# Kernel optimization log

Measured on AMD Instinct MI355X. Metric: run time of the kernel, lower is better.

## Reference

```python
import jax, jax.numpy as jnp
import numpy as np

# nuScenes-scale config: batch 2, 360x360 BEV grid (1440/4), 128 channels,
# 10 classes, 200 proposals, 3x3 NMS kernel, 40k occupied voxels per sample.
B, H, W_GRID, NUM_CLS, NUM_PROP, NMS_K = 2, 360, 360, 10, 200, 3
C = 128
N_PER_B = 40000
NEG_FILL = -1000000.0  # scatter_nd fill value from to_dense()


def _bev_pos():
    # replicates create_2D_grid: coord = (x_index_along_dim1, y_index_along_dim0)
    xs = jnp.arange(H, dtype=jnp.float32)
    ys = jnp.arange(W_GRID, dtype=jnp.float32)
    by, bx = jnp.meshgrid(xs, ys, indexing='ij')  # by[i,j]=i, bx[i,j]=j
    return jnp.stack([bx, by], axis=-1).reshape(-1, 2)  # [H*W, 2]


def setup_inputs() -> dict:
    key = jax.random.key(0)
    ks = jax.random.split(key, 10)
    # unique spatial locations per batch sample (sparse voxel coords)
    flats = [jax.random.permutation(ks[i], H * W_GRID)[:N_PER_B] for i in range(B)]
    flat = jnp.concatenate(flats)
    b = jnp.repeat(jnp.arange(B), N_PER_B)
    indices = jnp.stack([b, flat // W_GRID, flat % W_GRID], axis=1).astype(jnp.int32)
    features = jax.random.normal(ks[4], (B * N_PER_B, C), jnp.float32)
    # heatmap head (pointwise linears standing in for the submconv stack)
    W_hm1 = jax.random.normal(ks[5], (C, C), jnp.float32) * (2.0 / C) ** 0.5
    b_hm1 = jnp.zeros((C,), jnp.float32)
    W_hm2 = jax.random.normal(ks[6], (C, NUM_CLS), jnp.float32) * (2.0 / C) ** 0.5
    b_hm2 = jnp.full((NUM_CLS,), -2.19, jnp.float32)  # fc[-1].bias.fill_(-2.19)
    # class_encoding: nn.Conv1d(num_class, channels, 1)
    W_cls = jax.random.normal(ks[7], (C, NUM_CLS), jnp.float32) * 0.1
    b_cls = jnp.zeros((C,), jnp.float32)
    return dict(features=features, W_hm1=W_hm1, b_hm1=b_hm1, W_hm2=W_hm2,
                b_hm2=b_hm2, W_cls=W_cls, b_cls=b_cls, indices=indices)


def reference(features, W_hm1, b_hm1, W_hm2, b_hm2, W_cls, b_cls, indices):
    bidx, yi, xi = indices[:, 0], indices[:, 1], indices[:, 2]
    HW = H * W_GRID

    # --- x.dense(): scatter voxel features to dense BEV grid (zero fill) ---
    xd = jnp.zeros((B, H, W_GRID, C), features.dtype).at[bidx, yi, xi].set(features)
    x_flat = xd.reshape(B, HW, C).transpose(0, 2, 1)  # [B, C, HW]

    # --- heatmap head (per-voxel) then to_dense() with -1e6 fill ---
    hm = jax.nn.relu(features @ W_hm1 + b_hm1) @ W_hm2 + b_hm2  # [N, NUM_CLS]
    dense_hm = jnp.full((B, H, W_GRID, NUM_CLS), NEG_FILL, hm.dtype)
    dense_hm = dense_hm.at[bidx, yi, xi].set(hm).transpose(0, 3, 1, 2)  # [B,K,H,W]

    heat = jax.nn.sigmoid(dense_hm)  # detached in original

    # --- NMS-kernel peak extraction ---
    pad = NMS_K // 2
    inner = jax.lax.reduce_window(heat, -jnp.inf, jax.lax.max,
                                  (1, 1, NMS_K, NMS_K), (1, 1, 1, 1), 'VALID')
    local_max = jnp.zeros_like(heat).at[:, :, pad:H - pad, pad:W_GRID - pad].set(inner)
    # pedestrian (8) and traffic_cone (9): kernel size 1
    local_max = local_max.at[:, 8].set(heat[:, 8]).at[:, 9].set(heat[:, 9])
    heat = heat * (heat == local_max)
    heat_f = heat.reshape(B, NUM_CLS, HW)

    # --- top-k proposals over (class, location) ---
    _, top = jax.lax.top_k(heat_f.reshape(B, -1), NUM_PROP)  # [B, P]
    cls = top // HW
    idx = top % HW

    # --- gather proposal features + class encoding ---
    qf = jnp.take_along_axis(x_flat, jnp.broadcast_to(idx[:, None, :], (B, C, NUM_PROP)), axis=2)
    onehot = jax.nn.one_hot(cls, NUM_CLS, dtype=qf.dtype)  # [B, P, K]
    qf = qf + jnp.einsum('ck,bpk->bcp', W_cls, onehot) + b_cls[None, :, None]

    # --- proposal positions and heatmap scores ---
    query_pos = _bev_pos()[idx]  # [B, P, 2]
    qhs = jnp.take_along_axis(heat_f, jnp.broadcast_to(idx[:, None, :], (B, NUM_CLS, NUM_PROP)), axis=2)
    return qf, query_pos, qhs, cls
```

## Files before the change

### kernel.cpp

```cpp
#include <hip/hip_runtime.h>

#define HW 129600
#define WG 360
#define HG 360
#define NCLS 10
#define NPROP 200
#define CDIM 128
#define NROWS 80000
#define NB 2
#define NPB (NROWS / NB)
#define SEL_CAP 4096
#define HBINS 4096
#define RPB 64
#define PSTR 12

__device__ __forceinline__ void lds_cp16(float* l, const float* g) {
  __builtin_amdgcn_global_load_lds(
      (const __attribute__((address_space(1))) void*)g,
      (__attribute__((address_space(3))) void*)l, 16, 0, 0);
}

__device__ __forceinline__ float4 fmax4(float4 a, float4 b) {
  float4 r;
  r.x = fmaxf(a.x, b.x);
  r.y = fmaxf(a.y, b.y);
  r.z = fmaxf(a.z, b.z);
  r.w = fmaxf(a.w, b.w);
  return r;
}

__global__ __launch_bounds__(256, 4) void k_head(
    const float* __restrict__ feat, const float* __restrict__ W1,
    const float* __restrict__ b1, const float* __restrict__ W2,
    const float* __restrict__ b2, const int* __restrict__ idxs,
    float* __restrict__ val_raw, int* __restrict__ rowmap) {
  __shared__ __align__(16) float lds_w[2][16 * 128];
  __shared__ __align__(16) float lds_f[2][RPB * 16];
  const int tid = threadIdx.x;
  const int row0 = blockIdx.x * RPB;
  const int tc = tid & 31;
  const int tr = tid >> 5;
  const int wv = tid >> 6;
  const int lane = tid & 63;

  auto stage = [&](int kt, int nb) {
#pragma unroll
    for (int c = 0; c < 2; ++c) {
      const int off = (wv * 2 + c) * 256;
      lds_cp16(&lds_w[nb][off], W1 + kt * 2048 + off + lane * 4);
    }
    {
      const int off = wv * 256;
      const int fidx = off + lane * 4;
      const int r = fidx >> 4, kk = fidx & 15;
      lds_cp16(&lds_f[nb][off],
               feat + (size_t)(row0 + r) * CDIM + kt * 16 + kk);
    }
  };

  stage(0, 0);
  if (tid < RPB) {
    int row = row0 + tid;
    int bb = idxs[row * 3 + 0];
    int yy = idxs[row * 3 + 1];
    int xx = idxs[row * 3 + 2];
    rowmap[(size_t)bb * HW + yy * WG + xx] = row;
  }
  __syncthreads();

  float acc[8][4];
#pragma unroll
  for (int r = 0; r < 8; ++r)
#pragma unroll
    for (int c = 0; c < 4; ++c) acc[r][c] = 0.f;

  for (int kt = 0; kt < 8; ++kt) {
    const int cb = kt & 1;
    if (kt < 7) stage(kt + 1, cb ^ 1);
#pragma unroll
    for (int kg = 0; kg < 4; ++kg) {
      float4 w0 = *(const float4*)(&lds_w[cb][(kg * 4 + 0) * 128 + tc * 4]);
      float4 w1 = *(const float4*)(&lds_w[cb][(kg * 4 + 1) * 128 + tc * 4]);
      float4 w2 = *(const float4*)(&lds_w[cb][(kg * 4 + 2) * 128 + tc * 4]);
      float4 w3 = *(const float4*)(&lds_w[cb][(kg * 4 + 3) * 128 + tc * 4]);
#pragma unroll
      for (int r = 0; r < 8; ++r) {
        float4 fv = *(const float4*)(&lds_f[cb][(tr * 8 + r) * 16 + kg * 4]);
        acc[r][0] = fmaf(fv.x, w0.x, acc[r][0]);
        acc[r][0] = fmaf(fv.y, w1.x, acc[r][0]);
        acc[r][0] = fmaf(fv.z, w2.x, acc[r][0]);
        acc[r][0] = fmaf(fv.w, w3.x, acc[r][0]);
        acc[r][1] = fmaf(fv.x, w0.y, acc[r][1]);
        acc[r][1] = fmaf(fv.y, w1.y, acc[r][1]);
        acc[r][1] = fmaf(fv.z, w2.y, acc[r][1]);
        acc[r][1] = fmaf(fv.w, w3.y, acc[r][1]);
        acc[r][2] = fmaf(fv.x, w0.z, acc[r][2]);
        acc[r][2] = fmaf(fv.y, w1.z, acc[r][2]);
        acc[r][2] = fmaf(fv.z, w2.z, acc[r][2]);
        acc[r][2] = fmaf(fv.w, w3.z, acc[r][2]);
        acc[r][3] = fmaf(fv.x, w0.w, acc[r][3]);
        acc[r][3] = fmaf(fv.y, w1.w, acc[r][3]);
        acc[r][3] = fmaf(fv.z, w2.w, acc[r][3]);
        acc[r][3] = fmaf(fv.w, w3.w, acc[r][3]);
      }
    }
    __syncthreads();
  }

  float* w2t = &lds_f[0][0];
  for (int i = tid; i < CDIM * NCLS; i += 256) {
    int k = i / NCLS, j = i - k * NCLS;
    w2t[j * 128 + k] = W2[i];
  }
  __syncthreads();

  float* hbuf = &lds_w[0][0];
  float4 b1v = *(const float4*)(b1 + tc * 4);
#pragma unroll
  for (int half = 0; half < 2; ++half) {
    if ((tr >> 2) == half) {
      int ltr = tr & 3;
#pragma unroll
      for (int r = 0; r < 8; ++r) {
        float4 h;
        h.x = fmaxf(acc[r][0] + b1v.x, 0.f);
        h.y = fmaxf(acc[r][1] + b1v.y, 0.f);
        h.z = fmaxf(acc[r][2] + b1v.z, 0.f);
        h.w = fmaxf(acc[r][3] + b1v.w, 0.f);
        *(float4*)(hbuf + (ltr * 8 + r) * 128 + tc * 4) = h;
      }
    }
    __syncthreads();
    for (int o = tid; o < 32 * NCLS; o += 256) {
      int r = o / NCLS, j = o - r * NCLS;
      float s = b2[j];
      for (int i4 = 0; i4 < 32; ++i4) {
        int k4 = (i4 + tid) & 31;
        float4 hv = *(const float4*)(hbuf + r * 128 + k4 * 4);
        float4 wv2 = *(const float4*)(w2t + j * 128 + k4 * 4);
        s = fmaf(hv.x, wv2.x, s);
        s = fmaf(hv.y, wv2.y, s);
        s = fmaf(hv.z, wv2.z, s);
        s = fmaf(hv.w, wv2.w, s);
      }
      float heat = 1.0f / (1.0f + expf(-s));
      int gr = half * 32 + r;
      val_raw[(size_t)(row0 + gr) * PSTR + j] = heat;
    }
    __syncthreads();
  }
}

__global__ __launch_bounds__(256) void k_hist(
    const float* __restrict__ val_raw, const int* __restrict__ idxs,
    const int* __restrict__ rowmap, const float* __restrict__ zrow,
    float* __restrict__ val, unsigned int* __restrict__ hist) {
  __shared__ unsigned int lh[HBINS];
  const int tid = threadIdx.x;
  const int row = blockIdx.x * 256 + tid;
  const int blk_b = (blockIdx.x * 256 >= NPB) ? 1 : 0;
  for (int i = tid; i < HBINS; i += 256) lh[i] = 0;
  __syncthreads();

  float v[10];
  int bb = 0;
  const bool valid = row < NROWS;
  if (valid) {
    bb = (row >= NPB) ? 1 : 0;
    const int y = idxs[row * 3 + 1];
    const int x = idxs[row * 3 + 2];
    const int pos = y * WG + x;
    const float* cbase = val_raw + (size_t)row * PSTR;
    float4 c0 = *(const float4*)(cbase + 0);
    float4 c1 = *(const float4*)(cbase + 4);
    float2 c89 = *(const float2*)(cbase + 8);
    const bool interior = (y > 0 && y < HG - 1 && x > 0 && x < WG - 1);
    if (interior) {
      const int d[8] = {-1, 1, -WG - 1, -WG, -WG + 1, WG - 1, WG, WG + 1};
      float4 m0 = c0, m1 = c1;
      const int* rmb = rowmap + (size_t)bb * HW + pos;
#pragma unroll
      for (int n = 0; n < 8; ++n) {
        int nrow = rmb[d[n]];
        const float* p =
            (nrow >= 0) ? (val_raw + (size_t)nrow * PSTR) : zrow;
        m0 = fmax4(m0, *(const float4*)(p + 0));
        m1 = fmax4(m1, *(const float4*)(p + 4));
      }
      v[0] = (c0.x == m0.x) ? c0.x : 0.f;
      v[1] = (c0.y == m0.y) ? c0.y : 0.f;
      v[2] = (c0.z == m0.z) ? c0.z : 0.f;
      v[3] = (c0.w == m0.w) ? c0.w : 0.f;
      v[4] = (c1.x == m1.x) ? c1.x : 0.f;
      v[5] = (c1.y == m1.y) ? c1.y : 0.f;
      v[6] = (c1.z == m1.z) ? c1.z : 0.f;
      v[7] = (c1.w == m1.w) ? c1.w : 0.f;
    } else {
      v[0] = v[1] = v[2] = v[3] = v[4] = v[5] = v[6] = v[7] = 0.f;
    }
    v[8] = c89.x;
    v[9] = c89.y;
    float4 s0 = {v[0], v[1], v[2], v[3]};
    float4 s1 = {v[4], v[5], v[6], v[7]};
    float4 s2 = {v[8], v[9], 0.f, 0.f};
    *(float4*)(val + (size_t)row * PSTR + 0) = s0;
    *(float4*)(val + (size_t)row * PSTR + 4) = s1;
    *(float4*)(val + (size_t)row * PSTR + 8) = s2;
#pragma unroll
    for (int c = 0; c < 10; ++c) {
      if (v[c] > 0.f) {
        unsigned int bin = __float_as_uint(v[c]) >> 18;
        if (bb == blk_b)
          atomicAdd(&lh[bin], 1u);
        else
          atomicAdd(&hist[(size_t)bb * HBINS + bin], 1u);
      }
    }
  }
  __syncthreads();
  unsigned int* gh = hist + (size_t)blk_b * HBINS;
  for (int i = tid; i < HBINS; i += 256) {
    unsigned int c = lh[i];
    if (c) atomicAdd(&gh[i], c);
  }
}

__global__ __launch_bounds__(256) void k_collect(
    const float* __restrict__ val, const int* __restrict__ idxs,
    const unsigned int* __restrict__ hist, unsigned long long* __restrict__ sel,
    int* __restrict__ sel_cnt) {
  __shared__ unsigned int coarse[256];
  __shared__ int sT[2];
  const int tid = threadIdx.x;
  for (int bb = 0; bb < NB; ++bb) {
    const unsigned int* h = hist + (size_t)bb * HBINS;
    unsigned int s = 0;
#pragma unroll
    for (int i = 0; i < HBINS / 256; ++i) s += h[tid * (HBINS / 256) + i];
    coarse[tid] = s;
    __syncthreads();
    if (tid == 0) {
      unsigned int cum = 0;
      int T = 0;
      int ci = 255;
      for (; ci >= 0; --ci) {
        if (cum + coarse[ci] >= NPROP) break;
        cum += coarse[ci];
      }
      if (ci >= 0) {
        int t = 15;
        for (; t > 0; --t) {
          unsigned int c = h[ci * 16 + t];
          if (cum + c >= NPROP) break;
          cum += c;
        }
        T = ci * 16 + t;
      }
      sT[bb] = T;
    }
    __syncthreads();
  }
  const int row = blockIdx.x * 256 + tid;
  const bool valid = row < NROWS;
  const int bb = (valid && row >= NPB) ? 1 : 0;
  const int T = sT[bb];
  float v[12];
  int pos = 0;
  if (valid) {
    *(float4*)(v + 0) = *(const float4*)(val + (size_t)row * PSTR + 0);
    *(float4*)(v + 4) = *(const float4*)(val + (size_t)row * PSTR + 4);
    *(float4*)(v + 8) = *(const float4*)(val + (size_t)row * PSTR + 8);
    pos = idxs[row * 3 + 1] * WG + idxs[row * 3 + 2];
  }
  const int lane = tid & 63;
#pragma unroll
  for (int cl = 0; cl < 10; ++cl) {
    float vv = valid ? v[cl] : 0.f;
    unsigned int bits = __float_as_uint(vv);
    bool pred = (vv > 0.f) && ((int)(bits >> 18) >= T);
    unsigned long long m0 = __ballot(pred && (bb == 0));
    unsigned long long m1 = __ballot(pred && (bb == 1));
    if (pred) {
      unsigned long long mask = bb ? m1 : m0;
      int leader = __ffsll((unsigned long long)mask) - 1;
      int lb = __popcll(mask & ((1ull << lane) - 1ull));
      int base = 0;
      if (lane == leader) base = atomicAdd(&sel_cnt[bb], (int)__popcll(mask));
      base = __shfl(base, leader, 64);
      unsigned int gidx = (unsigned int)cl * HW + (unsigned int)pos;
      unsigned long long key =
          ((unsigned long long)bits << 32) | (unsigned long long)(~gidx);
      int slot = base + lb;
      if (slot < SEL_CAP) sel[(size_t)bb * SEL_CAP + slot] = key;
    }
  }
}

__global__ __launch_bounds__(256) void k_final(
    const unsigned long long* __restrict__ sel, const int* __restrict__ sel_cnt,
    const float* __restrict__ val, const int* __restrict__ rowmap,
    const float* __restrict__ feat, const float* __restrict__ Wc,
    const float* __restrict__ bc, float* __restrict__ out) {
  __shared__ unsigned long long sk[SEL_CAP];
  __shared__ unsigned long long winners[NPROP];
  __shared__ int wcls[NPROP];
  __shared__ int wrow[NPROP];
  const int b = blockIdx.x;
  const int tid = threadIdx.x;
  int M = sel_cnt[b];
  if (M > SEL_CAP) M = SEL_CAP;
  for (int i = tid; i < M; i += 256) sk[i] = sel[(size_t)b * SEL_CAP + i];
  __syncthreads();
  for (int i = tid; i < M; i += 256) {
    unsigned long long key = sk[i];
    int rank = 0;
    for (int j = 0; j < M; ++j) rank += (sk[j] > key) ? 1 : 0;
    if (rank < NPROP) winners[rank] = key;
  }
  __syncthreads();
  if (tid < NPROP) {
    unsigned long long key = winners[tid];
    unsigned int gidx = ~((unsigned int)(key & 0xFFFFFFFFull));
    int cls = (int)(gidx / HW);
    int pos = (int)(gidx - (unsigned int)cls * HW);
    int y = pos / WG, x = pos - y * WG;
    wcls[tid] = cls;
    wrow[tid] = rowmap[(size_t)b * HW + pos];
    out[51200 + ((size_t)b * NPROP + tid) * 2 + 0] = (float)x;
    out[51200 + ((size_t)b * NPROP + tid) * 2 + 1] = (float)y;
    out[56000 + b * NPROP + tid] = (float)cls;
  }
  __syncthreads();
  for (int o = tid; o < NCLS * NPROP; o += 256) {
    int j = o / NPROP, pp = o - j * NPROP;
    out[52000 + (size_t)b * NCLS * NPROP + o] = val[(size_t)wrow[pp] * PSTR + j];
  }
  for (int o = tid; o < CDIM * NPROP; o += 256) {
    int c = o / NPROP, pp = o - c * NPROP;
    out[(size_t)b * CDIM * NPROP + o] =
        feat[(size_t)wrow[pp] * CDIM + c] + Wc[c * NCLS + wcls[pp]] + bc[c];
  }
}

extern "C" void kernel_launch(void* const* d_in, const int* in_sizes, int n_in,
                              void* d_out, int out_size, void* d_ws,
                              size_t ws_size, hipStream_t stream) {
  const float* feat = (const float*)d_in[0];
  const float* W1 = (const float*)d_in[1];
  const float* b1 = (const float*)d_in[2];
  const float* W2 = (const float*)d_in[3];
  const float* b2 = (const float*)d_in[4];
  const float* Wc = (const float*)d_in[5];
  const float* bc = (const float*)d_in[6];
  const int* idxs = (const int*)d_in[7];
  float* out = (float*)d_out;

  char* ws = (char*)d_ws;
  float* zrow = (float*)(ws + 0);
  unsigned int* hist = (unsigned int*)(ws + 64);
  int* rowmap = (int*)(ws + 32832);
  unsigned long long* sel = (unsigned long long*)(ws + 1069632);
  int* sel_cnt = (int*)(ws + 1135168);
  float* val_raw = (float*)(ws + 1135184);
  float* val = (float*)(ws + 4975184);

  hipMemsetAsync(ws, 0, 64 + (size_t)NB * HBINS * sizeof(unsigned int),
                 stream);
  hipMemsetAsync(rowmap, 0xFF, (size_t)NB * HW * sizeof(int), stream);
  hipMemsetAsync(sel_cnt, 0, 2 * sizeof(int), stream);

  k_head<<<NROWS / RPB, 256, 0, stream>>>(feat, W1, b1, W2, b2, idxs, val_raw,
                                          rowmap);
  k_hist<<<(NROWS + 255) / 256, 256, 0, stream>>>(val_raw, idxs, rowmap, zrow,
                                                  val, hist);
  k_collect<<<(NROWS + 255) / 256, 256, 0, stream>>>(val, idxs, hist, sel,
                                                     sel_cnt);
  k_final<<<NB, 256, 0, stream>>>(sel, sel_cnt, val, rowmap, feat, Wc, bc, out);
}
```

Before: 196.0 us.

## Drop workspace memsets via validated rowmap lookups and parallelize threshold scan

Removes the three hipMemsetAsync calls. The histogram and selection counter are now zeroed by block 0 of the head kernel. The 1 MB rowmap initialization is skipped: neighbor lookups check that a stored row index is in range, in the right batch, and points back to the same coordinates in idxs. The zero row becomes a device constant. The top-k threshold search in k_collect replaces a serial scan over 256 coarse bins with a parallel suffix scan and vectorized histogram loads. The cost is extra idxs loads per neighbor in k_hist, in exchange for fewer launches and less memset traffic.

New measurement: 196.5 us. Within noise of the previous version (+0.2%).

```diff
diff --git a/kernel.cpp b/kernel.cpp
--- a/kernel.cpp
+++ b/kernel.cpp
@@ -14,6 +14,9 @@
 #define RPB 64
 #define PSTR 12
 
+__device__ __align__(16) const float ZROW[12] = {0.f, 0.f, 0.f, 0.f, 0.f, 0.f,
+                                                 0.f, 0.f, 0.f, 0.f, 0.f, 0.f};
+
 __device__ __forceinline__ void lds_cp16(float* l, const float* g) {
   __builtin_amdgcn_global_load_lds(
       (const __attribute__((address_space(1))) void*)g,
@@ -33,7 +36,8 @@
     const float* __restrict__ feat, const float* __restrict__ W1,
     const float* __restrict__ b1, const float* __restrict__ W2,
     const float* __restrict__ b2, const int* __restrict__ idxs,
-    float* __restrict__ val_raw, int* __restrict__ rowmap) {
+    float* __restrict__ val_raw, int* __restrict__ rowmap,
+    unsigned int* __restrict__ hist, int* __restrict__ sel_cnt) {
   __shared__ __align__(16) float lds_w[2][16 * 128];
   __shared__ __align__(16) float lds_f[2][RPB * 16];
   const int tid = threadIdx.x;
@@ -59,6 +63,12 @@
   };
 
   stage(0, 0);
+  if (blockIdx.x == 0) {
+    uint4* h4 = (uint4*)hist;
+    for (int i = tid; i < (NB * HBINS) / 4; i += 256)
+      h4[i] = make_uint4(0u, 0u, 0u, 0u);
+    if (tid < 2) sel_cnt[tid] = 0;
+  }
   if (tid < RPB) {
     int row = row0 + tid;
     int bb = idxs[row * 3 + 0];
@@ -153,8 +163,8 @@
 
 __global__ __launch_bounds__(256) void k_hist(
     const float* __restrict__ val_raw, const int* __restrict__ idxs,
-    const int* __restrict__ rowmap, const float* __restrict__ zrow,
-    float* __restrict__ val, unsigned int* __restrict__ hist) {
+    const int* __restrict__ rowmap, float* __restrict__ val,
+    unsigned int* __restrict__ hist) {
   __shared__ unsigned int lh[HBINS];
   const int tid = threadIdx.x;
   const int row = blockIdx.x * 256 + tid;
@@ -176,14 +186,20 @@
     float2 c89 = *(const float2*)(cbase + 8);
     const bool interior = (y > 0 && y < HG - 1 && x > 0 && x < WG - 1);
     if (interior) {
-      const int d[8] = {-1, 1, -WG - 1, -WG, -WG + 1, WG - 1, WG, WG + 1};
+      const int dyA[8] = {0, 0, -1, -1, -1, 1, 1, 1};
+      const int dxA[8] = {-1, 1, -1, 0, 1, -1, 0, 1};
       float4 m0 = c0, m1 = c1;
       const int* rmb = rowmap + (size_t)bb * HW + pos;
 #pragma unroll
       for (int n = 0; n < 8; ++n) {
-        int nrow = rmb[d[n]];
-        const float* p =
-            (nrow >= 0) ? (val_raw + (size_t)nrow * PSTR) : zrow;
+        const int nrow = rmb[dyA[n] * WG + dxA[n]];
+        bool ok =
+            ((unsigned)nrow < NROWS) && ((nrow >= NPB) == (bb == 1));
+        if (ok) {
+          ok = (idxs[nrow * 3 + 1] == y + dyA[n]) &&
+               (idxs[nrow * 3 + 2] == x + dxA[n]);
+        }
+        const float* p = ok ? (val_raw + (size_t)nrow * PSTR) : ZROW;
         m0 = fmax4(m0, *(const float4*)(p + 0));
         m1 = fmax4(m1, *(const float4*)(p + 4));
       }
@@ -230,33 +246,48 @@
     const unsigned int* __restrict__ hist, unsigned long long* __restrict__ sel,
     int* __restrict__ sel_cnt) {
   __shared__ unsigned int coarse[256];
+  __shared__ unsigned int fine16[16];
   __shared__ int sT[2];
+  __shared__ int sCi[2];
   const int tid = threadIdx.x;
   for (int bb = 0; bb < NB; ++bb) {
     const unsigned int* h = hist + (size_t)bb * HBINS;
+    const uint4* h4 = (const uint4*)(h + tid * 16);
     unsigned int s = 0;
 #pragma unroll
-    for (int i = 0; i < HBINS / 256; ++i) s += h[tid * (HBINS / 256) + i];
+    for (int i = 0; i < 4; ++i) {
+      uint4 q = h4[i];
+      s += q.x + q.y + q.z + q.w;
+    }
+    if (tid == 0) {
+      sCi[bb] = -1;
+      sT[bb] = 0;
+    }
     coarse[tid] = s;
     __syncthreads();
-    if (tid == 0) {
-      unsigned int cum = 0;
-      int T = 0;
-      int ci = 255;
-      for (; ci >= 0; --ci) {
-        if (cum + coarse[ci] >= NPROP) break;
-        cum += coarse[ci];
-      }
-      if (ci >= 0) {
+#pragma unroll
+    for (int off = 1; off < 256; off <<= 1) {
+      unsigned int vv = (tid + off < 256) ? coarse[tid + off] : 0u;
+      __syncthreads();
+      coarse[tid] += vv;
+      __syncthreads();
+    }
+    if (coarse[tid] >= NPROP) atomicMax(&sCi[bb], tid);
+    __syncthreads();
+    const int ci = sCi[bb];
+    if (ci >= 0) {
+      if (tid < 16) fine16[tid] = h[ci * 16 + tid];
+      __syncthreads();
+      if (tid == 0) {
+        unsigned int cum = (ci + 1 < 256) ? coarse[ci + 1] : 0u;
         int t = 15;
         for (; t > 0; --t) {
-          unsigned int c = h[ci * 16 + t];
+          unsigned int c = fine16[t];
           if (cum + c >= NPROP) break;
           cum += c;
         }
-        T = ci * 16 + t;
-      }
-      sT[bb] = T;
+        sT[bb] = ci * 16 + t;
+      }
     }
     __syncthreads();
   }
@@ -356,23 +387,17 @@
   float* out = (float*)d_out;
 
   char* ws = (char*)d_ws;
-  float* zrow = (float*)(ws + 0);
-  unsigned int* hist = (unsigned int*)(ws + 64);
-  int* rowmap = (int*)(ws + 32832);
-  unsigned long long* sel = (unsigned long long*)(ws + 1069632);
-  int* sel_cnt = (int*)(ws + 1135168);
-  float* val_raw = (float*)(ws + 1135184);
-  float* val = (float*)(ws + 4975184);
-
-  hipMemsetAsync(ws, 0, 64 + (size_t)NB * HBINS * sizeof(unsigned int),
-                 stream);
-  hipMemsetAsync(rowmap, 0xFF, (size_t)NB * HW * sizeof(int), stream);
-  hipMemsetAsync(sel_cnt, 0, 2 * sizeof(int), stream);
+  unsigned int* hist = (unsigned int*)(ws + 0);
+  int* rowmap = (int*)(ws + 32768);
+  unsigned long long* sel = (unsigned long long*)(ws + 1069568);
+  int* sel_cnt = (int*)(ws + 1135104);
+  float* val_raw = (float*)(ws + 1135120);
+  float* val = (float*)(ws + 4975120);
 
   k_head<<<NROWS / RPB, 256, 0, stream>>>(feat, W1, b1, W2, b2, idxs, val_raw,
-                                          rowmap);
-  k_hist<<<(NROWS + 255) / 256, 256, 0, stream>>>(val_raw, idxs, rowmap, zrow,
-                                                  val, hist);
+                                          rowmap, hist, sel_cnt);
+  k_hist<<<(NROWS + 255) / 256, 256, 0, stream>>>(val_raw, idxs, rowmap, val,
+                                                  hist);
   k_collect<<<(NROWS + 255) / 256, 256, 0, stream>>>(val, idxs, hist, sel,
                                                      sel_cnt);
   k_final<<<NB, 256, 0, stream>>>(sel, sel_cnt, val, rowmap, feat, Wc, bc, out);
```
